# Kernel tuning notes

Hardware: AMD Instinct MI355X
Metric: run time of the kernel (lower is better)

## Reference

```python
import jax, jax.numpy as jnp
import numpy as np

B, T, C = 2, 2048, 2048
H, KVH = 16, 4
HD = C // H            # head_dim = 128
REP = H // KVH         # q heads per kv head = 4


def _alibi_slopes(n_head):
    # get_slopes_power_of_2: start = 2^(-2^-(log2(H)-3)); s_h = start * start^h
    start = 2.0 ** (-(2.0 ** (-(np.log2(n_head) - 3.0))))
    return jnp.asarray([start ** (i + 1) for i in range(n_head)], jnp.float32)


def setup_inputs() -> dict:
    key = jax.random.key(0)
    ks = jax.random.split(key, 4)
    sc = 0.02
    return {
        "x": jax.random.normal(ks[0], (B, T, C), jnp.float32),
        "Wq": jax.random.normal(ks[1], (C, C), jnp.float32) * sc,
        "Wkv": jax.random.normal(ks[2], (C, HD * KVH * 2), jnp.float32) * sc,
        "Wo": jax.random.normal(ks[3], (C, C), jnp.float32) * sc,
        "bo": jnp.zeros((C,), jnp.float32),
    }


def reference(x, Wq, Wkv, Wo, bo):
    Bv, Tv, Cv = x.shape
    # projections
    q = (x @ Wq).reshape(Bv, Tv, H, HD).transpose(0, 2, 1, 3)      # (B,H,T,hd)
    k, v = jnp.split(x @ Wkv, 2, axis=-1)
    k = k.reshape(Bv, Tv, KVH, HD).transpose(0, 2, 1, 3)           # (B,KVH,T,hd)
    v = v.reshape(Bv, Tv, KVH, HD).transpose(0, 2, 1, 3)
    # torch .repeat tiles kv heads: query head h = r*KVH + g uses kv head g.
    qg = q.reshape(Bv, REP, KVH, Tv, HD)
    scores = jnp.einsum('brgtd,bgsd->brgts', qg, k) / jnp.sqrt(jnp.float32(HD))
    # ALiBi bias: tril((j - i) * slope_h), zero on/above diagonal region handled by causal mask
    idx = jnp.arange(Tv)
    diff = (idx[None, :] - idx[:, None]).astype(jnp.float32)       # j - i (negative below diag)
    slopes = _alibi_slopes(H).reshape(REP, KVH)                    # head h = r*KVH+g
    bias = jnp.tril(diff)[None, None] * slopes[:, :, None, None]   # (REP,KVH,T,T)
    causal = idx[None, :] <= idx[:, None]                          # (T,T)
    scores = jnp.where(causal[None, None, None], scores + bias[None], -jnp.inf)
    attn = jax.nn.softmax(scores, axis=-1)
    out = jnp.einsum('brgts,bgsd->brgtd', attn, v)                 # (B,REP,KVH,T,hd)
    out = out.reshape(Bv, H, Tv, HD).transpose(0, 2, 1, 3).reshape(Bv, Tv, Cv)
    return out @ Wo + bo
```

## Files before the change

### kernel.cpp

```cpp
#include <hip/hip_runtime.h>

typedef __attribute__((ext_vector_type(8))) __bf16 bf16x8;
typedef __attribute__((ext_vector_type(4))) float f32x4;

#define NEG_BIG (-1e30f)

__device__ __forceinline__ unsigned short f2b(float f) {
    unsigned int u = __float_as_uint(f);
    u += 0x7FFFu + ((u >> 16) & 1u);
    return (unsigned short)(u >> 16);
}
__device__ __forceinline__ float b2f(unsigned short h) {
    return __uint_as_float(((unsigned int)h) << 16);
}
__device__ __forceinline__ unsigned cvtpk(float lo, float hi) {
    unsigned r;
    asm("v_cvt_pk_bf16_f32 %0, %1, %2" : "=v"(r) : "v"(lo), "v"(hi));
    return r;
}

typedef const __attribute__((address_space(1))) unsigned int* gas_ptr;
typedef __attribute__((address_space(3))) unsigned int* las_ptr;
__device__ __forceinline__ void gload16(const void* g, void* l) {
    __builtin_amdgcn_global_load_lds((gas_ptr)g, (las_ptr)l, 16, 0, 0);
}

__global__ __launch_bounds__(256) void k_convert(
    const float* __restrict__ x, unsigned short* __restrict__ xb, int n4)
{
    int i = blockIdx.x * 256 + threadIdx.x;
    if (i >= n4) return;
    float4 v = reinterpret_cast<const float4*>(x)[i];
    ushort4 h;
    h.x = f2b(v.x); h.y = f2b(v.y); h.z = f2b(v.z); h.w = f2b(v.w);
    reinterpret_cast<ushort4*>(xb)[i] = h;
}

__global__ __launch_bounds__(256) void k_transpose(
    const float* __restrict__ W, unsigned short* __restrict__ Th, int K, int N)
{
    __shared__ float tile[64][65];
    const int n0 = blockIdx.x * 64, k0 = blockIdx.y * 64;
    const int c = threadIdx.x & 63, r0 = threadIdx.x >> 6;
    for (int rr = r0; rr < 64; rr += 4)
        tile[rr][c] = W[(size_t)(k0 + rr) * N + n0 + c];
    __syncthreads();
    for (int rr = r0; rr < 64; rr += 4)
        Th[(size_t)(n0 + rr) * K + k0 + c] = f2b(tile[c][rr]);
}

__global__ __launch_bounds__(256) void k_gemm(
    const unsigned short* __restrict__ A, const unsigned short* __restrict__ B,
    void* __restrict__ CoutA, int NA, void* __restrict__ CoutB, int NB, int N1,
    const float* __restrict__ bias, int M, int K, int outF32)
{
    __shared__ __align__(16) unsigned short As[128][32];
    __shared__ __align__(16) unsigned short Bs[128][32];

    const int tid  = threadIdx.x;
    const int lane = tid & 63, wid = tid >> 6;
    const int wr = wid >> 1, wc = wid & 1;
    const int lrow = lane & 15, lko = (lane >> 4) << 3;
    const int trow = tid >> 2, tk = (tid & 3) << 3;
    const int bm = blockIdx.y, bn = blockIdx.x;
    const int wbyte = wid * 1024;

    f32x4 acc[4][4] = {};

    const size_t aoff = (size_t)(bm * 128 + trow) * K + tk;
    const size_t boff = (size_t)(bn * 128 + trow) * K + tk;
    const size_t half = (size_t)64 * K;

    for (int k0 = 0; k0 < K; k0 += 32) {
        gload16(&A[aoff + k0],        (char*)&As[0][0] + wbyte);
        gload16(&A[aoff + half + k0], (char*)&As[0][0] + 4096 + wbyte);
        gload16(&B[boff + k0],        (char*)&Bs[0][0] + wbyte);
        gload16(&B[boff + half + k0], (char*)&Bs[0][0] + 4096 + wbyte);
        __syncthreads();

        bf16x8 af[4], bf[4];
        #pragma unroll
        for (int m = 0; m < 4; ++m)
            af[m] = *reinterpret_cast<const bf16x8*>(&As[wr * 64 + m * 16 + lrow][lko]);
        #pragma unroll
        for (int n = 0; n < 4; ++n)
            bf[n] = *reinterpret_cast<const bf16x8*>(&Bs[wc * 64 + n * 16 + lrow][lko]);
        #pragma unroll
        for (int m = 0; m < 4; ++m)
            #pragma unroll
            for (int n = 0; n < 4; ++n)
                acc[m][n] = __builtin_amdgcn_mfma_f32_16x16x32_bf16(af[m], bf[n], acc[m][n], 0, 0, 0);
        __syncthreads();
    }

    const int rbase = bm * 128 + wr * 64 + ((lane >> 4) << 2);
    const int cbase = bn * 128 + wc * 64 + lrow;
    #pragma unroll
    for (int m = 0; m < 4; ++m)
        #pragma unroll
        for (int n = 0; n < 4; ++n) {
            const int col = cbase + n * 16;
            const float bv = bias ? bias[col] : 0.0f;
            const bool inA = (col < N1);
            const int ccol = inA ? col : (col - N1);
            const int cstr = inA ? NA : NB;
            void* base = inA ? CoutA : CoutB;
            #pragma unroll
            for (int r = 0; r < 4; ++r) {
                const size_t idx = (size_t)(rbase + m * 16 + r) * cstr + ccol;
                const float v = acc[m][n][r] + bv;
                if (outF32) ((float*)base)[idx] = v;
                else        ((unsigned short*)base)[idx] = f2b(v);
            }
        }
}

__global__ __launch_bounds__(512, 4) void k_attn(
    const unsigned short* __restrict__ Qb,
    const unsigned short* __restrict__ KVb,
    unsigned short* __restrict__ AO)
{
    __shared__ __align__(16) unsigned short Ksl[64][128];
    __shared__ __align__(16) unsigned short Vt[128][72];
    __shared__ __align__(16) unsigned short Psl[8][16][72];

    const int blk = blockIdx.x;
    const int idx = blk >> 3;
    const int sub = blk & 7;
    const int b   = sub >> 2;
    const int g   = sub & 3;
    const int chunk = (idx < 32) ? (63 - idx) : (idx - 32);
    const int q0  = chunk * 32;

    const int tid = threadIdx.x;
    const int lane = tid & 63;
    const int w = tid >> 6;
    const int h = (w & 3) * 4 + g;
    const int q0w = q0 + (w >> 2) * 16;
    const float slope = exp2f(-0.5f * (float)(h + 1));
    const float isq = 0.088388347648318447f;
    const int lrow = lane & 15;
    const int lko  = (lane >> 4) << 3;
    const int rowg = (lane >> 4) << 2;
    const int skey = tid >> 4;
    const int sd0  = (tid & 15) << 3;
    const int vdim = tid & 127;
    const int vkg  = tid >> 7;

    uint4 kreg[2];
    unsigned short vv[2][8];

    auto ldK = [&](int kb) {
        const int j0 = kb << 6;
        #pragma unroll
        for (int pp = 0; pp < 2; ++pp) {
            const int key = skey + pp * 32;
            kreg[pp] = *reinterpret_cast<const uint4*>(
                &KVb[(size_t)(b * 2048 + j0 + key) * 1024 + g * 128 + sd0]);
        }
    };
    auto wrK = [&]() {
        #pragma unroll
        for (int pp = 0; pp < 2; ++pp) {
            const int key = skey + pp * 32;
            *reinterpret_cast<uint4*>(&Ksl[key][sd0 ^ ((key & 7) << 3)]) = kreg[pp];
        }
    };
    auto ldV = [&](int kb) {
        const int j0 = kb << 6;
        #pragma unroll
        for (int gi = 0; gi < 2; ++gi) {
            const int kgi = gi * 4 + vkg;
            const size_t base = (size_t)(b * 2048 + j0 + kgi * 8) * 1024 + 512 + g * 128 + vdim;
            #pragma unroll
            for (int j = 0; j < 8; ++j)
                vv[gi][j] = KVb[base + (size_t)j * 1024];
        }
    };
    auto wrV = [&]() {
        #pragma unroll
        for (int gi = 0; gi < 2; ++gi) {
            const int kgi = gi * 4 + vkg;
            *reinterpret_cast<uint4*>(&Vt[vdim][kgi * 8]) =
                *reinterpret_cast<const uint4*>(&vv[gi][0]);
        }
    };

    bf16x8 qf[4];
    {
        const size_t qoff = (size_t)(b * 2048 + q0w + lrow) * 2048 + h * 128 + lko;
        #pragma unroll
        for (int kk = 0; kk < 4; ++kk)
            qf[kk] = *reinterpret_cast<const bf16x8*>(&Qb[qoff + kk * 32]);
    }

    f32x4 oacc[8] = {};
    float mrow = NEG_BIG, lsum = 0.f;
    const int nkb = (q0 + 32 + 63) >> 6;
    const int q = q0w + lrow;

    ldK(0); ldV(0);
    wrK(); wrV();
    __syncthreads();

    for (int kb = 0; kb < nkb; ++kb) {
        const int j0 = kb << 6;
        const bool pre = (kb + 1 < nkb);
        if (pre) { ldK(kb + 1); ldV(kb + 1); }

        f32x4 sa[4] = {};
        #pragma unroll
        for (int c = 0; c < 4; ++c) {
            const int krow = c * 16 + lrow;
            #pragma unroll
            for (int kk = 0; kk < 4; ++kk) {
                bf16x8 kf = *reinterpret_cast<const bf16x8*>(
                    &Ksl[krow][(kk * 32 + lko) ^ ((krow & 7) << 3)]);
                sa[c] = __builtin_amdgcn_mfma_f32_16x16x32_bf16(kf, qf[kk], sa[c], 0, 0, 0);
            }
        }

        float pv[4][4];
        float mt = NEG_BIG;
        #pragma unroll
        for (int c = 0; c < 4; ++c)
            #pragma unroll
            for (int r = 0; r < 4; ++r) {
                const int j = j0 + c * 16 + rowg + r;
                const float vsc = (j <= q) ? (sa[c][r] * isq + slope * (float)(j - q)) : NEG_BIG;
                pv[c][r] = vsc;
                mt = fmaxf(mt, vsc);
            }
        mt = fmaxf(mt, __shfl_xor(mt, 16));
        mt = fmaxf(mt, __shfl_xor(mt, 32));
        const float mn = fmaxf(mrow, mt);
        const float alpha = __expf(mrow - mn);
        mrow = mn;
        float s = 0.f;
        #pragma unroll
        for (int c = 0; c < 4; ++c)
            #pragma unroll
            for (int r = 0; r < 4; ++r) {
                const float pe = __expf(pv[c][r] - mn);
                pv[c][r] = pe;
                s += pe;
            }
        s += __shfl_xor(s, 16);
        s += __shfl_xor(s, 32);
        lsum = lsum * alpha + s;

        float ar[4];
        #pragma unroll
        for (int r = 0; r < 4; ++r) ar[r] = __shfl(alpha, rowg + r);
        #pragma unroll
        for (int f = 0; f < 8; ++f)
            #pragma unroll
            for (int r = 0; r < 4; ++r)
                oacc[f][r] *= ar[r];

        #pragma unroll
        for (int c = 0; c < 4; ++c) {
            uint2 pw;
            pw.x = cvtpk(pv[c][0], pv[c][1]);
            pw.y = cvtpk(pv[c][2], pv[c][3]);
            *reinterpret_cast<uint2*>(&Psl[w][lrow][c * 16 + rowg]) = pw;
        }
        asm volatile("s_waitcnt lgkmcnt(0)" ::: "memory");

        #pragma unroll
        for (int kk2 = 0; kk2 < 2; ++kk2) {
            bf16x8 pf = *reinterpret_cast<const bf16x8*>(&Psl[w][lrow][kk2 * 32 + lko]);
            #pragma unroll
            for (int nb = 0; nb < 8; ++nb) {
                bf16x8 vf = *reinterpret_cast<const bf16x8*>(&Vt[nb * 16 + lrow][kk2 * 32 + lko]);
                oacc[nb] = __builtin_amdgcn_mfma_f32_16x16x32_bf16(pf, vf, oacc[nb], 0, 0, 0);
            }
        }

        __syncthreads();
        if (pre) { wrK(); wrV(); }
        __syncthreads();
    }

    float lr[4];
    #pragma unroll
    for (int r = 0; r < 4; ++r) lr[r] = __shfl(lsum, rowg + r);
    #pragma unroll
    for (int nb = 0; nb < 8; ++nb)
        #pragma unroll
        for (int r = 0; r < 4; ++r) {
            const int row = q0w + rowg + r;
            const int col = h * 128 + nb * 16 + lrow;
            const float vo = oacc[nb][r] / lr[r];
            AO[(size_t)(b * 2048 + row) * 2048 + col] = f2b(vo);
        }
}

extern "C" void kernel_launch(void* const* d_in, const int* in_sizes, int n_in,
                              void* d_out, int out_size, void* d_ws, size_t ws_size,
                              hipStream_t stream)
{
    const float* x   = (const float*)d_in[0];
    const float* Wq  = (const float*)d_in[1];
    const float* Wkv = (const float*)d_in[2];
    const float* Wo  = (const float*)d_in[3];
    const float* bo  = (const float*)d_in[4];

    char* ws = (char*)d_ws;
    unsigned short* xb  = (unsigned short*)(ws + (size_t)0);
    unsigned short* Wt  = (unsigned short*)(ws + ((size_t)16 << 20));
    unsigned short* Qb  = (unsigned short*)(ws + ((size_t)28 << 20));
    unsigned short* KVb = (unsigned short*)(ws + ((size_t)44 << 20));

    k_convert<<<8192, 256, 0, stream>>>(x, xb, (2 * 2048 * 2048) / 4);

    k_transpose<<<dim3(32, 32), 256, 0, stream>>>(Wq, Wt, 2048, 2048);
    k_transpose<<<dim3(16, 32), 256, 0, stream>>>(Wkv, Wt + (size_t)2048 * 2048, 2048, 1024);

    k_gemm<<<dim3(24, 32), 256, 0, stream>>>(xb, Wt, Qb, 2048, KVb, 1024, 2048,
                                             nullptr, 4096, 2048, 0);

    k_attn<<<512, 512, 0, stream>>>(Qb, KVb, xb);

    k_transpose<<<dim3(32, 32), 256, 0, stream>>>(Wo, Wt, 2048, 2048);
    k_gemm<<<dim3(16, 32), 256, 0, stream>>>(xb, Wt, d_out, 2048, nullptr, 2048, 2048,
                                             bo, 4096, 2048, 1);
}
```

Measured before the change: 262.8 us.

## Use exp2 domain, precomputed ALiBi offsets, mask-free full blocks and lazy rescale

Folds log2(e) into the score scale and ALiBi slope so the softmax can use exp2 directly. It also precomputes the per-lane ALiBi offsets once, skips causal masking for key blocks that lie entirely below the diagonal, and skips the running-max update and accumulator rescale when no row's max grows by more than a threshold (the FA4-style lazy rescale). This cuts VALU work in the softmax section of the attention loop. In exchange it adds wave-wide branching, and it relies on bounded growth of the exponent when the max is not updated.

```diff
diff --git a/kernel.cpp b/kernel.cpp
--- a/kernel.cpp
+++ b/kernel.cpp
@@ -137,8 +137,8 @@
     const int w = tid >> 6;
     const int h = (w & 3) * 4 + g;
     const int q0w = q0 + (w >> 2) * 16;
-    const float slope = exp2f(-0.5f * (float)(h + 1));
-    const float isq = 0.088388347648318447f;
+    const float slope2 = exp2f(-0.5f * (float)(h + 1)) * 1.4426950408889634f;
+    const float isq2 = 0.088388347648318447f * 1.4426950408889634f;
     const int lrow = lane & 15;
     const int lko  = (lane >> 4) << 3;
     const int rowg = (lane >> 4) << 2;
@@ -199,6 +199,13 @@
     const int nkb = (q0 + 32 + 63) >> 6;
     const int q = q0w + lrow;
 
+    float offs[4][4];
+    #pragma unroll
+    for (int c = 0; c < 4; ++c)
+        #pragma unroll
+        for (int r = 0; r < 4; ++r)
+            offs[c][r] = slope2 * (float)(c * 16 + rowg + r);
+
     ldK(0); ldV(0);
     wrK(); wrV();
     __syncthreads();
@@ -220,43 +227,70 @@
             }
         }
 
+        const float base_b = slope2 * (float)(j0 - q);
+        const int qmj0 = q - j0;
         float pv[4][4];
         float mt = NEG_BIG;
-        #pragma unroll
-        for (int c = 0; c < 4; ++c)
-            #pragma unroll
-            for (int r = 0; r < 4; ++r) {
-                const int j = j0 + c * 16 + rowg + r;
-                const float vsc = (j <= q) ? (sa[c][r] * isq + slope * (float)(j - q)) : NEG_BIG;
-                pv[c][r] = vsc;
-                mt = fmaxf(mt, vsc);
-            }
+        if (j0 + 63 <= q0w) {
+            #pragma unroll
+            for (int c = 0; c < 4; ++c)
+                #pragma unroll
+                for (int r = 0; r < 4; ++r) {
+                    const float vsc = fmaf(sa[c][r], isq2, base_b + offs[c][r]);
+                    pv[c][r] = vsc;
+                    mt = fmaxf(mt, vsc);
+                }
+        } else {
+            #pragma unroll
+            for (int c = 0; c < 4; ++c)
+                #pragma unroll
+                for (int r = 0; r < 4; ++r) {
+                    const float vsc = (c * 16 + rowg + r <= qmj0)
+                        ? fmaf(sa[c][r], isq2, base_b + offs[c][r]) : NEG_BIG;
+                    pv[c][r] = vsc;
+                    mt = fmaxf(mt, vsc);
+                }
+        }
         mt = fmaxf(mt, __shfl_xor(mt, 16));
         mt = fmaxf(mt, __shfl_xor(mt, 32));
-        const float mn = fmaxf(mrow, mt);
-        const float alpha = __expf(mrow - mn);
-        mrow = mn;
+
         float s = 0.f;
-        #pragma unroll
-        for (int c = 0; c < 4; ++c)
-            #pragma unroll
-            for (int r = 0; r < 4; ++r) {
-                const float pe = __expf(pv[c][r] - mn);
-                pv[c][r] = pe;
-                s += pe;
-            }
-        s += __shfl_xor(s, 16);
-        s += __shfl_xor(s, 32);
-        lsum = lsum * alpha + s;
-
-        float ar[4];
-        #pragma unroll
-        for (int r = 0; r < 4; ++r) ar[r] = __shfl(alpha, rowg + r);
-        #pragma unroll
-        for (int f = 0; f < 8; ++f)
-            #pragma unroll
-            for (int r = 0; r < 4; ++r)
-                oacc[f][r] *= ar[r];
+        if (__all(mt - mrow <= 12.0f)) {
+            #pragma unroll
+            for (int c = 0; c < 4; ++c)
+                #pragma unroll
+                for (int r = 0; r < 4; ++r) {
+                    const float pe = exp2f(pv[c][r] - mrow);
+                    pv[c][r] = pe;
+                    s += pe;
+                }
+            s += __shfl_xor(s, 16);
+            s += __shfl_xor(s, 32);
+            lsum += s;
+        } else {
+            const float mn = fmaxf(mrow, mt);
+            const float alpha = exp2f(mrow - mn);
+            mrow = mn;
+            #pragma unroll
+            for (int c = 0; c < 4; ++c)
+                #pragma unroll
+                for (int r = 0; r < 4; ++r) {
+                    const float pe = exp2f(pv[c][r] - mn);
+                    pv[c][r] = pe;
+                    s += pe;
+                }
+            s += __shfl_xor(s, 16);
+            s += __shfl_xor(s, 32);
+            lsum = lsum * alpha + s;
+            float ar[4];
+            #pragma unroll
+            for (int r = 0; r < 4; ++r) ar[r] = __shfl(alpha, rowg + r);
+            #pragma unroll
+            for (int f = 0; f < 8; ++f)
+                #pragma unroll
+                for (int r = 0; r < 4; ++r)
+                    oacc[f][r] *= ar[r];
+        }
 
         #pragma unroll
         for (int c = 0; c < 4; ++c) {
```

Result: slower. 540.0 us (+105.5%).
